# Optimization experiments

Measured on AMD Instinct MI355X. Metric: run time of the kernel, lower is better.

The kernel has to match this reference:

```python
import jax, jax.numpy as jnp
import numpy as np

B, M, H, E = 1, 2048, 16, 128
D = H * E          # 2048, model dim
C = 4 * D          # 8192, FFN dim
F = E
G = D
J = D


def setup_inputs() -> dict:
    key = jax.random.key(0)
    k_in, k_wv, k_wk, k_wq, k_wz, k_ffa, k_ffb = jax.random.split(key, 7)
    scale = 0.01
    return {
        "I_in": jax.random.normal(k_in, (B, M, D), dtype=jnp.float32),
        "WV": jax.random.normal(k_wv, (H, E, D), dtype=jnp.float32) * scale,
        "WK": jax.random.normal(k_wk, (H, E, D), dtype=jnp.float32) * scale,
        "WQ": jax.random.normal(k_wq, (H, E, D), dtype=jnp.float32) * scale,
        "WZ": jax.random.normal(k_wz, (H, F, G), dtype=jnp.float32) * scale,
        "WFFA": jax.random.normal(k_ffa, (G, C), dtype=jnp.float32) * scale,
        "WFFB": jax.random.normal(k_ffb, (C, J), dtype=jnp.float32) * scale,
    }


def reference(I_in, WV, WK, WQ, WZ, WFFA, WFFB):
    # QKV projections: [B,M,D] x [H,E,D] -> [B,M,H,E]
    V = jnp.einsum('bmd,hed->bmhe', I_in, WV)
    K = jnp.einsum('bmd,hed->bmhe', I_in, WK)
    Q = jnp.einsum('bmd,hed->bmhe', I_in, WQ)
    # Attention scores [B,M,P,H]; NOTE: no 1/sqrt(E) scaling in the original.
    QK = jnp.einsum('bmhe,bphe->bmph', Q, K)
    # Softmax over keys (p axis = 2), matching torch.softmax(QK, dim=2)
    QK_softmax = jax.nn.softmax(QK, axis=2)
    # Attention output [B,M,H,E]
    AV = jnp.einsum('bmph,bphe->bmhe', QK_softmax, V)
    # Output projection [B,M,G]
    Z = jnp.einsum('bmhf,hfg->bmg', AV, WZ)
    # FFN (no nonlinearity in the original workload)
    FFA = jnp.einsum('bmg,gc->bmc', Z, WFFA)
    FFB = jnp.einsum('bmc,cj->bmj', FFA, WFFB)
    return FFB
```

## Files before the change

kernel.cpp:

```cpp
#include <hip/hip_runtime.h>
#include <hip/hip_bf16.h>
#include <math.h>


typedef __bf16 bf16_t;
typedef __bf16 bf16x8 __attribute__((ext_vector_type(8)));
typedef float  f32x4  __attribute__((ext_vector_type(4)));

#define AS1 __attribute__((address_space(1)))
#define AS3 __attribute__((address_space(3)))

__device__ __forceinline__ void load16_lds(const bf16_t* g, bf16_t* l) {
    __builtin_amdgcn_global_load_lds((AS1 void*)g, (AS3 void*)l, 16, 0, 0);
}

template<typename TOUT, bool ATOMIC>
__global__ __launch_bounds__(256)
void gemm_bt(const bf16_t* __restrict__ A, const bf16_t* __restrict__ B,
             TOUT* __restrict__ Cc, int Mdim, int Ndim, int Kdim,
             int lda, int ldb, int ldc,
             long long ab, long long bb, long long cb,
             int ct_z, bf16_t* __restrict__ ctc, int ldct)
{
    __shared__ bf16_t As[128 * 32];
    __shared__ bf16_t Bs[128 * 32];

    const int z = blockIdx.z;
    A  += (long long)z * ab;
    B  += (long long)z * bb;
    Cc += (long long)z * cb;

    const int bm = blockIdx.y * 128;
    const int bn = blockIdx.x * 128;
    const int t  = threadIdx.x;
    const int lane = t & 63;
    const int w    = t >> 6;

    const int wm = (w & 1) * 64;
    const int wn = (w >> 1) * 64;

    const int sub = lane >> 2;
    const int seg = lane & 3;

    const bf16_t* Ag0 = A + (long long)(bm + w * 32 + sub) * lda + seg * 8;
    const bf16_t* Ag1 = Ag0 + 16LL * lda;
    const bf16_t* Bg0 = B + (long long)(bn + w * 32 + sub) * ldb + seg * 8;
    const bf16_t* Bg1 = Bg0 + 16LL * ldb;

    bf16_t* Al0 = &As[(w * 2 + 0) * 512];
    bf16_t* Al1 = &As[(w * 2 + 1) * 512];
    bf16_t* Bl0 = &Bs[(w * 2 + 0) * 512];
    bf16_t* Bl1 = &Bs[(w * 2 + 1) * 512];

    const int col  = lane & 15;
    const int koff = (lane >> 4) * 8;

    f32x4 acc[4][4] = {};

    for (int k0 = 0; k0 < Kdim; k0 += 32) {
        load16_lds(Ag0 + k0, Al0);
        load16_lds(Ag1 + k0, Al1);
        load16_lds(Bg0 + k0, Bl0);
        load16_lds(Bg1 + k0, Bl1);
        __syncthreads();

        bf16x8 af[4], bfr[4];
        #pragma unroll
        for (int mi = 0; mi < 4; ++mi)
            af[mi] = *(const bf16x8*)&As[(wm + mi * 16 + col) * 32 + koff];
        #pragma unroll
        for (int nj = 0; nj < 4; ++nj)
            bfr[nj] = *(const bf16x8*)&Bs[(wn + nj * 16 + col) * 32 + koff];
        #pragma unroll
        for (int mi = 0; mi < 4; ++mi)
            #pragma unroll
            for (int nj = 0; nj < 4; ++nj)
                acc[mi][nj] = __builtin_amdgcn_mfma_f32_16x16x32_bf16(
                    af[mi], bfr[nj], acc[mi][nj], 0, 0, 0);
        __syncthreads();
    }

    const int rbase = (lane >> 4) * 4;
    if (z == ct_z) {
        #pragma unroll
        for (int mi = 0; mi < 4; ++mi) {
            const long long mb = bm + wm + mi * 16 + rbase;
            #pragma unroll
            for (int nj = 0; nj < 4; ++nj) {
                const long long n = bn + wn + nj * 16 + col;
                union { bf16_t b[4]; unsigned long long u; } o;
                #pragma unroll
                for (int r = 0; r < 4; ++r) o.b[r] = (bf16_t)acc[mi][nj][r];
                *(unsigned long long*)(ctc + n * ldct + mb) = o.u;
            }
        }
    } else {
        #pragma unroll
        for (int mi = 0; mi < 4; ++mi) {
            #pragma unroll
            for (int r = 0; r < 4; ++r) {
                long long m = bm + wm + mi * 16 + rbase + r;
                TOUT* crow = Cc + m * ldc + bn + wn + col;
                #pragma unroll
                for (int nj = 0; nj < 4; ++nj) {
                    if constexpr (ATOMIC)
                        atomicAdd(&crow[nj * 16], (float)acc[mi][nj][r]);
                    else
                        crow[nj * 16] = (TOUT)acc[mi][nj][r];
                }
            }
        }
    }
}

__global__ __launch_bounds__(256, 2)
void flash_attn(const bf16_t* __restrict__ Q, const bf16_t* __restrict__ K,
                const bf16_t* __restrict__ VT, bf16_t* __restrict__ O,
                int M, int D)
{
    __shared__ bf16_t Kt[64 * 128];
    __shared__ bf16_t Vt[128 * 64];
    __shared__ bf16_t Pl[4 * 16 * 88];

    const int t = threadIdx.x, lane = t & 63, w = t >> 6;
    const int q4 = lane >> 4;
    const int c  = lane & 15;
    const int bm = blockIdx.x * 64;
    const int hE = blockIdx.y * 128;

    bf16x8 af_q[4];
    {
        const bf16_t* qrow = Q + (long long)(bm + w * 16 + c) * D + hE + q4 * 8;
        #pragma unroll
        for (int ks = 0; ks < 4; ++ks)
            af_q[ks] = *(const bf16x8*)(qrow + ks * 32);
    }

    f32x4 acc_o[8] = {};
    float m_i[4] = {-INFINITY, -INFINITY, -INFINITY, -INFINITY};
    float l_i[4] = {0.f, 0.f, 0.f, 0.f};

    bf16_t* Pw = &Pl[w * 16 * 88];

    for (int p0 = 0; p0 < M; p0 += 64) {
        #pragma unroll
        for (int j = 0; j < 4; ++j) {
            int krow = w * 16 + j * 4;
            load16_lds(K + (long long)(p0 + krow + q4) * D + hE + ((c ^ (j * 4 + q4)) * 8),
                       &Kt[krow * 128]);
            int vrow = w * 32 + j * 8;
            load16_lds(VT + (long long)(hE + vrow + (lane >> 3)) * M + p0
                          + (((lane & 7) ^ (lane >> 3)) * 8),
                       &Vt[vrow * 64]);
        }
        __syncthreads();

        f32x4 acc_s[4] = {};
        #pragma unroll
        for (int ks = 0; ks < 4; ++ks) {
            #pragma unroll
            for (int nj = 0; nj < 4; ++nj) {
                int row = nj * 16 + c;
                bf16x8 bk = *(const bf16x8*)&Kt[row * 128 + (((ks * 4 + q4) ^ c) * 8)];
                acc_s[nj] = __builtin_amdgcn_mfma_f32_16x16x32_bf16(
                    af_q[ks], bk, acc_s[nj], 0, 0, 0);
            }
        }

        float mt[4], alpha[4], rs[4];
        #pragma unroll
        for (int r = 0; r < 4; ++r) {
            float v = fmaxf(fmaxf(acc_s[0][r], acc_s[1][r]),
                            fmaxf(acc_s[2][r], acc_s[3][r]));
            #pragma unroll
            for (int off = 1; off < 16; off <<= 1)
                v = fmaxf(v, __shfl_xor(v, off));
            mt[r] = v;
        }
        #pragma unroll
        for (int r = 0; r < 4; ++r) {
            float mn = fmaxf(m_i[r], mt[r]);
            alpha[r] = __expf(m_i[r] - mn);
            m_i[r] = mn;
            rs[r] = 0.f;
        }
        #pragma unroll
        for (int nj = 0; nj < 4; ++nj)
            #pragma unroll
            for (int r = 0; r < 4; ++r) {
                float p = __expf(acc_s[nj][r] - m_i[r]);
                rs[r] += p;
                Pw[(q4 * 4 + r) * 88 + nj * 16 + c] = (bf16_t)p;
            }
        #pragma unroll
        for (int r = 0; r < 4; ++r) {
            float v = rs[r];
            #pragma unroll
            for (int off = 1; off < 16; off <<= 1)
                v += __shfl_xor(v, off);
            l_i[r] = alpha[r] * l_i[r] + v;
        }
        #pragma unroll
        for (int nj = 0; nj < 8; ++nj)
            #pragma unroll
            for (int r = 0; r < 4; ++r)
                acc_o[nj][r] *= alpha[r];
        __syncthreads();

        #pragma unroll
        for (int ks = 0; ks < 2; ++ks) {
            bf16x8 ap = *(const bf16x8*)&Pw[c * 88 + ks * 32 + q4 * 8];
            #pragma unroll
            for (int nj = 0; nj < 8; ++nj) {
                int row = nj * 16 + c;
                bf16x8 bv = *(const bf16x8*)&Vt[row * 64 + (((ks * 4 + q4) ^ (c & 7)) * 8)];
                acc_o[nj] = __builtin_amdgcn_mfma_f32_16x16x32_bf16(
                    ap, bv, acc_o[nj], 0, 0, 0);
            }
        }
        __syncthreads();
    }

    float inv[4];
    #pragma unroll
    for (int r = 0; r < 4; ++r) inv[r] = 1.0f / l_i[r];
    #pragma unroll
    for (int nj = 0; nj < 8; ++nj)
        #pragma unroll
        for (int r = 0; r < 4; ++r)
            O[(long long)(bm + w * 16 + q4 * 4 + r) * D + hE + nj * 16 + c] =
                (bf16_t)(acc_o[nj][r] * inv[r]);
}

__global__ __launch_bounds__(256)
void cast4_bf16(const float* __restrict__ s0, const float* __restrict__ s1,
                const float* __restrict__ s2, const float* __restrict__ s3,
                bf16_t* __restrict__ d0, long long seg, long long n)
{
    const float* src = (blockIdx.y == 0) ? s0 : (blockIdx.y == 1) ? s1
                     : (blockIdx.y == 2) ? s2 : s3;
    bf16_t* dst = d0 + (long long)blockIdx.y * seg;
    long long i = ((long long)blockIdx.x * 256 + threadIdx.x) * 4;
    if (i >= n) return;
    float4 v = *(const float4*)(src + i);
    union { bf16_t b[4]; unsigned long long u; } o;
    o.b[0] = (bf16_t)v.x; o.b[1] = (bf16_t)v.y;
    o.b[2] = (bf16_t)v.z; o.b[3] = (bf16_t)v.w;
    *(unsigned long long*)(dst + i) = o.u;
}

__global__ __launch_bounds__(256)
void transpose_to_bf16(const float* __restrict__ in, bf16_t* __restrict__ out,
                       int rows, int cols)
{
    __shared__ bf16_t tile[32][33];
    const int r0 = blockIdx.y * 32, c0 = blockIdx.x * 32;
    const int tx = threadIdx.x & 31, ty = threadIdx.x >> 5;
    #pragma unroll
    for (int i = 0; i < 4; ++i) {
        int r = ty + i * 8;
        tile[r][tx] = (bf16_t)in[(long long)(r0 + r) * cols + c0 + tx];
    }
    __syncthreads();
    #pragma unroll
    for (int i = 0; i < 4; ++i) {
        int r = ty + i * 8;
        out[(long long)(c0 + r) * rows + r0 + tx] = tile[tx][r];
    }
}

__global__ __launch_bounds__(256)
void zero_f32(float* __restrict__ p, long long n)
{
    long long i = ((long long)blockIdx.x * 256 + threadIdx.x) * 4;
    if (i >= n) return;
    *(float4*)(p + i) = float4{0.f, 0.f, 0.f, 0.f};
}

extern "C" void kernel_launch(void* const* d_in, const int* in_sizes, int n_in,
                              void* d_out, int out_size, void* d_ws, size_t ws_size,
                              hipStream_t stream)
{
    const float* I    = (const float*)d_in[0];
    const float* WV   = (const float*)d_in[1];
    const float* WK   = (const float*)d_in[2];
    const float* WQ   = (const float*)d_in[3];
    const float* WZ   = (const float*)d_in[4];
    const float* WFFA = (const float*)d_in[5];
    const float* WFFB = (const float*)d_in[6];
    float* out = (float*)d_out;

    const int M = 2048, D = 2048, C = 8192;
    const long long MD = (long long)M * D;
    const size_t MiB = 1024 * 1024;

    char* base = (char*)d_ws;
    bf16_t* bI     = (bf16_t*)(base + 0 * MiB);
    bf16_t* bWQ    = (bf16_t*)(base + 8 * MiB);
    bf16_t* bWK    = (bf16_t*)(base + 16 * MiB);
    bf16_t* bWV    = (bf16_t*)(base + 24 * MiB);
    bf16_t* bQ     = (bf16_t*)(base + 32 * MiB);
    bf16_t* bK     = (bf16_t*)(base + 40 * MiB);
    bf16_t* bVT    = (bf16_t*)(base + 48 * MiB);
    bf16_t* bAV    = (bf16_t*)(base + 56 * MiB);
    bf16_t* bZ     = (bf16_t*)(base + 64 * MiB);
    bf16_t* bWZT   = (bf16_t*)(base + 72 * MiB);
    bf16_t* bWFFAT = (bf16_t*)(base + 80 * MiB);
    bf16_t* bWFFBT = (bf16_t*)(base + 112 * MiB);
    bf16_t* bFFA   = (bf16_t*)(base + 0 * MiB);

    const dim3 blk(256);

    cast4_bf16<<<dim3(MD / 1024, 4), blk, 0, stream>>>(I, WQ, WK, WV, bI, MD, MD);
    transpose_to_bf16<<<dim3(D / 32, D / 32), blk, 0, stream>>>(WZ,   bWZT,   D, D);
    transpose_to_bf16<<<dim3(C / 32, D / 32), blk, 0, stream>>>(WFFA, bWFFAT, D, C);
    transpose_to_bf16<<<dim3(D / 32, C / 32), blk, 0, stream>>>(WFFB, bWFFBT, C, D);

    gemm_bt<bf16_t, false><<<dim3(16, 16, 3), blk, 0, stream>>>(
        bI, bWQ, bQ, M, D, D, D, D, D, 0, MD, MD, 2, bVT, M);

    flash_attn<<<dim3(M / 64, 16), blk, 0, stream>>>(bQ, bK, bVT, bAV, M, D);

    gemm_bt<bf16_t, false><<<dim3(16, 16, 1), blk, 0, stream>>>(
        bAV, bWZT, bZ, M, D, D, D, D, D, 0, 0, 0, -1, nullptr, 0);

    gemm_bt<bf16_t, false><<<dim3(64, 16, 1), blk, 0, stream>>>(
        bZ, bWFFAT, bFFA, M, C, D, D, D, C, 0, 0, 0, -1, nullptr, 0);

    zero_f32<<<dim3((int)(MD / 1024)), blk, 0, stream>>>(out, MD);
    gemm_bt<float, true><<<dim3(16, 16, 4), blk, 0, stream>>>(
        bFFA, bWFFBT, out, M, D, 2048, C, C, D, 2048, 2048, 0, -1, nullptr, 0);
}
```

Baseline: 690.3 us.

## Add 256x256 double-buffered GEMM kernel with swizzled LDS for large projections

Introduces a 512-thread GEMM kernel with 256x256 output tiles and 64-wide K steps. It double-buffers LDS, uses XOR-swizzled loads to avoid bank conflicts, and interleaves the next tile's async global-to-LDS loads with MFMA phases, raising MFMA priority during compute. The kernel replaces the 128x128 GEMM for the QKV, FFN-A and split-K FFN-B stages, aiming for more data reuse and better latency hiding. The cost is much more LDS (128KB per block) and more registers, which lowers occupancy and gives fewer blocks per grid (e.g. 192 for QKV).

```diff
diff --git a/kernel.cpp b/kernel.cpp
--- a/kernel.cpp
+++ b/kernel.cpp
@@ -12,6 +12,172 @@
 
 __device__ __forceinline__ void load16_lds(const bf16_t* g, bf16_t* l) {
     __builtin_amdgcn_global_load_lds((AS1 void*)g, (AS3 void*)l, 16, 0, 0);
+}
+
+
+__device__ __forceinline__ void stageA256(const bf16_t* __restrict__ Ab, int lda,
+                                          int k0, bf16_t* buf, int half,
+                                          int w, int lane)
+{
+    #pragma unroll
+    for (int j = 0; j < 2; ++j) {
+        const int prw = half * 128 + j * 64 + w * 8;
+        const int pr  = prw + (lane >> 3);
+        const int lr  = ((pr >> 6) & 1) * 128 + (pr >> 7) * 64 + (pr & 63);
+        const int lc  = (lane & 7) ^ (pr & 7);
+        load16_lds(Ab + (long long)lr * lda + k0 + lc * 8, buf + prw * 64);
+    }
+}
+
+__device__ __forceinline__ void stageB256(const bf16_t* __restrict__ Bb, int ldb,
+                                          int k0, bf16_t* buf, int half,
+                                          int w, int lane)
+{
+    #pragma unroll
+    for (int j = 0; j < 2; ++j) {
+        const int prw = half * 128 + j * 64 + w * 8;
+        const int pr  = prw + (lane >> 3);
+        const int lr  = ((pr >> 5) & 3) * 64 + (pr >> 7) * 32 + (pr & 31);
+        const int lc  = (lane & 7) ^ (pr & 7);
+        load16_lds(Bb + (long long)lr * ldb + k0 + lc * 8, buf + prw * 64);
+    }
+}
+
+#define G256_PHASE(MH, NH, DOA, DOB, STAGE, WAIT)                              \
+  {                                                                            \
+    if constexpr (DOA) {                                                       \
+      const int arow_ = (MH) * 128 + wm * 64 + (lane & 15);                    \
+      _Pragma("unroll")                                                        \
+      for (int ks = 0; ks < 2; ++ks) {                                         \
+        const int ch_ = (((ks * 4 + (lane >> 4)) ^ (lane & 7)) * 8);           \
+        _Pragma("unroll")                                                      \
+        for (int mi = 0; mi < 4; ++mi)                                         \
+          af[ks][mi] = *(const bf16x8*)&Ac[(arow_ + mi * 16) * 64 + ch_];      \
+      }                                                                        \
+    }                                                                          \
+    if constexpr (DOB) {                                                       \
+      const int brow_ = (NH) * 128 + wn * 32 + (lane & 15);                    \
+      _Pragma("unroll")                                                        \
+      for (int ks = 0; ks < 2; ++ks) {                                         \
+        const int ch_ = (((ks * 4 + (lane >> 4)) ^ (lane & 7)) * 8);           \
+        _Pragma("unroll")                                                      \
+        for (int nj = 0; nj < 2; ++nj)                                         \
+          bv[ks][nj] = *(const bf16x8*)&Bc[(brow_ + nj * 16) * 64 + ch_];      \
+      }                                                                        \
+    }                                                                          \
+    STAGE;                                                                     \
+    WAIT;                                                                      \
+    __builtin_amdgcn_s_barrier();                                              \
+    asm volatile("s_waitcnt lgkmcnt(0)" ::: "memory");                         \
+    __builtin_amdgcn_s_setprio(1);                                             \
+    _Pragma("unroll")                                                          \
+    for (int ks = 0; ks < 2; ++ks)                                             \
+      _Pragma("unroll")                                                        \
+      for (int mi = 0; mi < 4; ++mi)                                           \
+        _Pragma("unroll")                                                      \
+        for (int nj = 0; nj < 2; ++nj)                                         \
+          acc[(MH) * 4 + mi][(NH) * 2 + nj] =                                  \
+              __builtin_amdgcn_mfma_f32_16x16x32_bf16(                         \
+                  af[ks][mi], bv[ks][nj],                                      \
+                  acc[(MH) * 4 + mi][(NH) * 2 + nj], 0, 0, 0);                 \
+    __builtin_amdgcn_s_setprio(0);                                             \
+    __builtin_amdgcn_s_barrier();                                              \
+  }
+
+template<typename TOUT, bool ATOMIC>
+__global__ __launch_bounds__(512, 2)
+void gemm256_bt(const bf16_t* __restrict__ A, const bf16_t* __restrict__ B,
+                TOUT* __restrict__ Cc, int Kdim,
+                int lda, int ldb, int ldc,
+                long long ab, long long bb, long long cb,
+                int ct_z, bf16_t* __restrict__ ctc, int ldct)
+{
+    __shared__ __attribute__((aligned(16))) bf16_t Asl[2][256 * 64];
+    __shared__ __attribute__((aligned(16))) bf16_t Bsl[2][256 * 64];
+
+    const int z = blockIdx.z;
+    A  += (long long)z * ab;
+    B  += (long long)z * bb;
+    Cc += (long long)z * cb;
+
+    const int bm = blockIdx.y * 256;
+    const int bn = blockIdx.x * 256;
+    const int t = threadIdx.x, lane = t & 63, w = t >> 6;
+    const int wm = w >> 2, wn = w & 3;
+
+    const bf16_t* Ab = A + (long long)bm * lda;
+    const bf16_t* Bb = B + (long long)bn * ldb;
+
+    f32x4  acc[8][4] = {};
+    bf16x8 af[2][4];
+    bf16x8 bv[2][2];
+
+    stageA256(Ab, lda, 0, &Asl[0][0], 0, w, lane);
+    stageB256(Bb, ldb, 0, &Bsl[0][0], 0, w, lane);
+    stageA256(Ab, lda, 0, &Asl[0][0], 1, w, lane);
+    stageB256(Bb, ldb, 0, &Bsl[0][0], 1, w, lane);
+    asm volatile("s_waitcnt vmcnt(4)" ::: "memory");
+    __builtin_amdgcn_s_barrier();
+
+    const int NT = Kdim >> 6;
+    for (int kt = 0; kt < NT - 1; ++kt) {
+        const int cur = kt & 1, nxt = cur ^ 1;
+        const int k0n = (kt + 1) << 6;
+        const bf16_t* Ac = &Asl[cur][0];
+        const bf16_t* Bc = &Bsl[cur][0];
+        G256_PHASE(0, 0, 1, 1, stageA256(Ab, lda, k0n, &Asl[nxt][0], 0, w, lane),
+                   asm volatile("s_waitcnt vmcnt(4)" ::: "memory"));
+        G256_PHASE(1, 0, 1, 0, stageB256(Bb, ldb, k0n, &Bsl[nxt][0], 0, w, lane),
+                   asm volatile("s_waitcnt vmcnt(4)" ::: "memory"));
+        G256_PHASE(1, 1, 0, 1, stageA256(Ab, lda, k0n, &Asl[nxt][0], 1, w, lane),
+                   ((void)0));
+        G256_PHASE(0, 1, 1, 0, stageB256(Bb, ldb, k0n, &Bsl[nxt][0], 1, w, lane),
+                   asm volatile("s_waitcnt vmcnt(4)" ::: "memory"));
+    }
+    {
+        const int cur = (NT - 1) & 1;
+        const bf16_t* Ac = &Asl[cur][0];
+        const bf16_t* Bc = &Bsl[cur][0];
+        G256_PHASE(0, 0, 1, 1, ((void)0),
+                   asm volatile("s_waitcnt vmcnt(2)" ::: "memory"));
+        G256_PHASE(1, 0, 1, 0, ((void)0),
+                   asm volatile("s_waitcnt vmcnt(0)" ::: "memory"));
+        G256_PHASE(1, 1, 0, 1, ((void)0), ((void)0));
+        G256_PHASE(0, 1, 1, 0, ((void)0), ((void)0));
+    }
+
+    const int rb = (lane >> 4) * 4;
+    const int cc = lane & 15;
+    if (z == ct_z) {
+        #pragma unroll
+        for (int mi = 0; mi < 8; ++mi) {
+            const long long mb = bm + wm * 128 + mi * 16 + rb;
+            #pragma unroll
+            for (int nj = 0; nj < 4; ++nj) {
+                const long long n = bn + wn * 64 + nj * 16 + cc;
+                union { bf16_t b[4]; unsigned long long u; } o;
+                #pragma unroll
+                for (int r = 0; r < 4; ++r) o.b[r] = (bf16_t)acc[mi][nj][r];
+                *(unsigned long long*)(ctc + n * ldct + mb) = o.u;
+            }
+        }
+    } else {
+        #pragma unroll
+        for (int mi = 0; mi < 8; ++mi) {
+            #pragma unroll
+            for (int r = 0; r < 4; ++r) {
+                const long long m = bm + wm * 128 + mi * 16 + rb + r;
+                TOUT* crow = Cc + m * ldc + bn + wn * 64 + cc;
+                #pragma unroll
+                for (int nj = 0; nj < 4; ++nj) {
+                    if constexpr (ATOMIC)
+                        atomicAdd(&crow[nj * 16], (float)acc[mi][nj][r]);
+                    else
+                        crow[nj * 16] = (TOUT)acc[mi][nj][r];
+                }
+            }
+        }
+    }
 }
 
 template<typename TOUT, bool ATOMIC>
@@ -64,10 +230,10 @@
         load16_lds(Bg1 + k0, Bl1);
         __syncthreads();
 
-        bf16x8 af[4], bfr[4];
+        bf16x8 afr[4], bfr[4];
         #pragma unroll
         for (int mi = 0; mi < 4; ++mi)
-            af[mi] = *(const bf16x8*)&As[(wm + mi * 16 + col) * 32 + koff];
+            afr[mi] = *(const bf16x8*)&As[(wm + mi * 16 + col) * 32 + koff];
         #pragma unroll
         for (int nj = 0; nj < 4; ++nj)
             bfr[nj] = *(const bf16x8*)&Bs[(wn + nj * 16 + col) * 32 + koff];
@@ -76,7 +242,7 @@
             #pragma unroll
             for (int nj = 0; nj < 4; ++nj)
                 acc[mi][nj] = __builtin_amdgcn_mfma_f32_16x16x32_bf16(
-                    af[mi], bfr[nj], acc[mi][nj], 0, 0, 0);
+                    afr[mi], bfr[nj], acc[mi][nj], 0, 0, 0);
         __syncthreads();
     }
 
@@ -213,9 +379,9 @@
             #pragma unroll
             for (int nj = 0; nj < 8; ++nj) {
                 int row = nj * 16 + c;
-                bf16x8 bv = *(const bf16x8*)&Vt[row * 64 + (((ks * 4 + q4) ^ (c & 7)) * 8)];
+                bf16x8 bvv = *(const bf16x8*)&Vt[row * 64 + (((ks * 4 + q4) ^ (c & 7)) * 8)];
                 acc_o[nj] = __builtin_amdgcn_mfma_f32_16x16x32_bf16(
-                    ap, bv, acc_o[nj], 0, 0, 0);
+                    ap, bvv, acc_o[nj], 0, 0, 0);
             }
         }
         __syncthreads();
@@ -310,24 +476,25 @@
     bf16_t* bFFA   = (bf16_t*)(base + 0 * MiB);
 
     const dim3 blk(256);
+    const dim3 blk512(512);
 
     cast4_bf16<<<dim3(MD / 1024, 4), blk, 0, stream>>>(I, WQ, WK, WV, bI, MD, MD);
     transpose_to_bf16<<<dim3(D / 32, D / 32), blk, 0, stream>>>(WZ,   bWZT,   D, D);
     transpose_to_bf16<<<dim3(C / 32, D / 32), blk, 0, stream>>>(WFFA, bWFFAT, D, C);
     transpose_to_bf16<<<dim3(D / 32, C / 32), blk, 0, stream>>>(WFFB, bWFFBT, C, D);
 
-    gemm_bt<bf16_t, false><<<dim3(16, 16, 3), blk, 0, stream>>>(
-        bI, bWQ, bQ, M, D, D, D, D, D, 0, MD, MD, 2, bVT, M);
+    gemm256_bt<bf16_t, false><<<dim3(8, 8, 3), blk512, 0, stream>>>(
+        bI, bWQ, bQ, D, D, D, D, 0, MD, MD, 2, bVT, M);
 
     flash_attn<<<dim3(M / 64, 16), blk, 0, stream>>>(bQ, bK, bVT, bAV, M, D);
 
     gemm_bt<bf16_t, false><<<dim3(16, 16, 1), blk, 0, stream>>>(
         bAV, bWZT, bZ, M, D, D, D, D, D, 0, 0, 0, -1, nullptr, 0);
 
-    gemm_bt<bf16_t, false><<<dim3(64, 16, 1), blk, 0, stream>>>(
-        bZ, bWFFAT, bFFA, M, C, D, D, D, C, 0, 0, 0, -1, nullptr, 0);
+    gemm256_bt<bf16_t, false><<<dim3(32, 8, 1), blk512, 0, stream>>>(
+        bZ, bWFFAT, bFFA, D, D, D, C, 0, 0, 0, -1, nullptr, 0);
 
     zero_f32<<<dim3((int)(MD / 1024)), blk, 0, stream>>>(out, MD);
-    gemm_bt<float, true><<<dim3(16, 16, 4), blk, 0, stream>>>(
-        bFFA, bWFFBT, out, M, D, 2048, C, C, D, 2048, 2048, 0, -1, nullptr, 0);
-}
+    gemm256_bt<float, true><<<dim3(8, 8, 4), blk512, 0, stream>>>(
+        bFFA, bWFFBT, out, 2048, C, C, D, 2048, 2048, 0, -1, nullptr, 0);
+}
```

After: 691.7 us. Within noise of the previous version (+0.2%).

## Add 256x256 pipelined GEMM kernel and replace atomic split-K with partial-sum reduction

Applied to the files above, without the earlier changes.

Introduces a 512-thread GEMM with 256x256 tiles, K-step 64, XOR-swizzled LDS, multi-buffered async global-to-LDS staging with explicit vmcnt waits, and MFMA priority bumps. It is used for the QKV projection and both FFN GEMMs, cutting global and LDS traffic per FLOP and overlapping loads with compute. The FFB split-K no longer zeroes the output and accumulates atomically. It writes four fp32 partial buffers that a separate kernel sums, at the cost of extra workspace traffic. The larger tiles give fewer blocks (e.g. 192 or 256), which may leave some of the GPU's compute units underused.

```diff
diff --git a/kernel.cpp b/kernel.cpp
--- a/kernel.cpp
+++ b/kernel.cpp
@@ -12,6 +12,189 @@
 
 __device__ __forceinline__ void load16_lds(const bf16_t* g, bf16_t* l) {
     __builtin_amdgcn_global_load_lds((AS1 void*)g, (AS3 void*)l, 16, 0, 0);
+}
+
+__device__ __forceinline__ void stageA_half(const bf16_t* __restrict__ Ab, int lda,
+                                            int k0, int h, bf16_t* slot,
+                                            int w, int lane)
+{
+    #pragma unroll
+    for (int j = 0; j < 2; ++j) {
+        const int prw = j * 64 + w * 8;
+        const int p   = prw + (lane >> 3);
+        const int lr  = (p >> 6) * 128 + h * 64 + (p & 63);
+        const int lc  = (lane & 7) ^ (p & 7);
+        load16_lds(Ab + (long long)lr * lda + k0 + lc * 8, slot + prw * 64);
+    }
+}
+__device__ __forceinline__ void stageB_half(const bf16_t* __restrict__ Bb, int ldb,
+                                            int k0, int h, bf16_t* slot,
+                                            int w, int lane)
+{
+    #pragma unroll
+    for (int j = 0; j < 2; ++j) {
+        const int prw = j * 64 + w * 8;
+        const int p   = prw + (lane >> 3);
+        const int lr  = (p >> 5) * 64 + h * 32 + (p & 31);
+        const int lc  = (lane & 7) ^ (p & 7);
+        load16_lds(Bb + (long long)lr * ldb + k0 + lc * 8, slot + prw * 64);
+    }
+}
+
+#define LOADAF(SL)                                                             \
+  _Pragma("unroll") for (int ks = 0; ks < 2; ++ks)                             \
+  _Pragma("unroll") for (int mi = 0; mi < 4; ++mi)                             \
+      af[ks][mi] = *(const bf16x8*)&(SL)[(wm * 64 + mi * 16 + c15) * 64 +      \
+                      (((ks * 4 + q4) ^ (c15 & 7)) * 8)];
+
+#define LOADBV(DST, SL)                                                        \
+  _Pragma("unroll") for (int ks = 0; ks < 2; ++ks)                             \
+  _Pragma("unroll") for (int nj = 0; nj < 2; ++nj)                             \
+      DST[ks][nj] = *(const bf16x8*)&(SL)[(wn * 32 + nj * 16 + c15) * 64 +     \
+                      (((ks * 4 + q4) ^ (c15 & 7)) * 8)];
+
+#define MFMA16(MH, NH, BV)                                                     \
+  __builtin_amdgcn_s_setprio(1);                                               \
+  _Pragma("unroll") for (int ks = 0; ks < 2; ++ks)                             \
+  _Pragma("unroll") for (int mi = 0; mi < 4; ++mi)                             \
+  _Pragma("unroll") for (int nj = 0; nj < 2; ++nj)                             \
+      acc[(MH) * 4 + mi][(NH) * 2 + nj] =                                      \
+          __builtin_amdgcn_mfma_f32_16x16x32_bf16(                             \
+              af[ks][mi], BV[ks][nj], acc[(MH) * 4 + mi][(NH) * 2 + nj],       \
+              0, 0, 0);                                                        \
+  __builtin_amdgcn_s_setprio(0);
+
+#define VMW(N) asm volatile("s_waitcnt vmcnt(" #N ")" ::: "memory")
+#define BAR()  __builtin_amdgcn_s_barrier()
+
+template<typename TOUT>
+__global__ __launch_bounds__(512, 2)
+void gemm256d_bt(const bf16_t* __restrict__ A, const bf16_t* __restrict__ B,
+                 TOUT* __restrict__ Cc, int Kdim,
+                 int lda, int ldb, int ldc,
+                 long long ab, long long bb, long long cb,
+                 int ct_z, bf16_t* __restrict__ ctc, int ldct)
+{
+    __shared__ __attribute__((aligned(16))) bf16_t As[4][128 * 64];
+    __shared__ __attribute__((aligned(16))) bf16_t Bs[4][128 * 64];
+
+    const int z = blockIdx.z;
+    A  += (long long)z * ab;
+    B  += (long long)z * bb;
+    Cc += (long long)z * cb;
+
+    const int bm = blockIdx.y * 256;
+    const int bn = blockIdx.x * 256;
+    const int t = threadIdx.x, lane = t & 63, w = t >> 6;
+    const int wm = w >> 2, wn = w & 3;
+    const int q4 = lane >> 4, c15 = lane & 15;
+
+    const bf16_t* Ab = A + (long long)bm * lda;
+    const bf16_t* Bb = B + (long long)bn * ldb;
+
+    f32x4  acc[8][4] = {};
+    bf16x8 af[2][4];
+    bf16x8 bv0[2][2];
+    bf16x8 bv1[2][2];
+
+    stageA_half(Ab, lda, 0,  0, As[0], w, lane);
+    stageB_half(Bb, ldb, 0,  0, Bs[0], w, lane);
+    stageB_half(Bb, ldb, 0,  1, Bs[1], w, lane);
+    stageA_half(Ab, lda, 0,  1, As[1], w, lane);
+    stageA_half(Ab, lda, 64, 0, As[2], w, lane);
+    stageB_half(Bb, ldb, 64, 0, Bs[2], w, lane);
+    stageB_half(Bb, ldb, 64, 1, Bs[3], w, lane);
+
+    const int NT = Kdim >> 6;
+
+    for (int kt = 0; kt + 2 < NT; ++kt) {
+        const int par = kt & 1;
+        bf16_t* a0 = As[2 * par];
+        bf16_t* a1 = As[2 * par + 1];
+        bf16_t* b0 = Bs[2 * par];
+        bf16_t* b1 = Bs[2 * par + 1];
+        bf16_t* a1n = As[2 * (par ^ 1) + 1];
+        const int kn1 = (kt + 1) << 6, kn2 = (kt + 2) << 6;
+        VMW(10); BAR();
+        stageA_half(Ab, lda, kn1, 1, a1n, w, lane);
+        LOADAF(a0); LOADBV(bv0, b0);
+        MFMA16(0, 0, bv0);
+        VMW(10); BAR();
+        LOADBV(bv1, b1);
+        MFMA16(0, 1, bv1);
+        VMW(8); BAR();
+        stageA_half(Ab, lda, kn2, 0, a0, w, lane);
+        stageB_half(Bb, ldb, kn2, 0, b0, w, lane);
+        LOADAF(a1);
+        MFMA16(1, 1, bv1);
+        stageB_half(Bb, ldb, kn2, 1, b1, w, lane);
+        MFMA16(1, 0, bv0);
+    }
+    {
+        const int kt = NT - 2, par = kt & 1;
+        bf16_t* a0 = As[2 * par];
+        bf16_t* a1 = As[2 * par + 1];
+        bf16_t* b0 = Bs[2 * par];
+        bf16_t* b1 = Bs[2 * par + 1];
+        bf16_t* a1n = As[2 * (par ^ 1) + 1];
+        const int kn1 = (kt + 1) << 6;
+        VMW(10); BAR();
+        stageA_half(Ab, lda, kn1, 1, a1n, w, lane);
+        LOADAF(a0); LOADBV(bv0, b0);
+        MFMA16(0, 0, bv0);
+        VMW(10); BAR();
+        LOADBV(bv1, b1);
+        MFMA16(0, 1, bv1);
+        VMW(8); BAR();
+        LOADAF(a1);
+        MFMA16(1, 1, bv1);
+        MFMA16(1, 0, bv0);
+    }
+    {
+        const int par = (NT - 1) & 1;
+        bf16_t* a0 = As[2 * par];
+        bf16_t* a1 = As[2 * par + 1];
+        bf16_t* b0 = Bs[2 * par];
+        bf16_t* b1 = Bs[2 * par + 1];
+        VMW(4); BAR();
+        LOADAF(a0); LOADBV(bv0, b0);
+        MFMA16(0, 0, bv0);
+        VMW(2); BAR();
+        LOADBV(bv1, b1);
+        MFMA16(0, 1, bv1);
+        VMW(0); BAR();
+        LOADAF(a1);
+        MFMA16(1, 1, bv1);
+        MFMA16(1, 0, bv0);
+    }
+
+    const int rb = q4 * 4;
+    if (z == ct_z) {
+        #pragma unroll
+        for (int mi = 0; mi < 8; ++mi) {
+            const long long mb = bm + wm * 128 + mi * 16 + rb;
+            #pragma unroll
+            for (int nj = 0; nj < 4; ++nj) {
+                const long long n = bn + wn * 64 + nj * 16 + c15;
+                union { bf16_t b[4]; unsigned long long u; } o;
+                #pragma unroll
+                for (int r = 0; r < 4; ++r) o.b[r] = (bf16_t)acc[mi][nj][r];
+                *(unsigned long long*)(ctc + n * ldct + mb) = o.u;
+            }
+        }
+    } else {
+        #pragma unroll
+        for (int mi = 0; mi < 8; ++mi) {
+            #pragma unroll
+            for (int r = 0; r < 4; ++r) {
+                const long long m = bm + wm * 128 + mi * 16 + rb + r;
+                TOUT* crow = Cc + m * ldc + bn + wn * 64 + c15;
+                #pragma unroll
+                for (int nj = 0; nj < 4; ++nj)
+                    crow[nj * 16] = (TOUT)acc[mi][nj][r];
+            }
+        }
+    }
 }
 
 template<typename TOUT, bool ATOMIC>
@@ -22,8 +205,8 @@
              long long ab, long long bb, long long cb,
              int ct_z, bf16_t* __restrict__ ctc, int ldct)
 {
-    __shared__ bf16_t As[128 * 32];
-    __shared__ bf16_t Bs[128 * 32];
+    __shared__ bf16_t Ash[128 * 32];
+    __shared__ bf16_t Bsh[128 * 32];
 
     const int z = blockIdx.z;
     A  += (long long)z * ab;
@@ -47,10 +230,10 @@
     const bf16_t* Bg0 = B + (long long)(bn + w * 32 + sub) * ldb + seg * 8;
     const bf16_t* Bg1 = Bg0 + 16LL * ldb;
 
-    bf16_t* Al0 = &As[(w * 2 + 0) * 512];
-    bf16_t* Al1 = &As[(w * 2 + 1) * 512];
-    bf16_t* Bl0 = &Bs[(w * 2 + 0) * 512];
-    bf16_t* Bl1 = &Bs[(w * 2 + 1) * 512];
+    bf16_t* Al0 = &Ash[(w * 2 + 0) * 512];
+    bf16_t* Al1 = &Ash[(w * 2 + 1) * 512];
+    bf16_t* Bl0 = &Bsh[(w * 2 + 0) * 512];
+    bf16_t* Bl1 = &Bsh[(w * 2 + 1) * 512];
 
     const int col  = lane & 15;
     const int koff = (lane >> 4) * 8;
@@ -64,19 +247,19 @@
         load16_lds(Bg1 + k0, Bl1);
         __syncthreads();
 
-        bf16x8 af[4], bfr[4];
+        bf16x8 afr[4], bfr[4];
         #pragma unroll
         for (int mi = 0; mi < 4; ++mi)
-            af[mi] = *(const bf16x8*)&As[(wm + mi * 16 + col) * 32 + koff];
+            afr[mi] = *(const bf16x8*)&Ash[(wm + mi * 16 + col) * 32 + koff];
         #pragma unroll
         for (int nj = 0; nj < 4; ++nj)
-            bfr[nj] = *(const bf16x8*)&Bs[(wn + nj * 16 + col) * 32 + koff];
+            bfr[nj] = *(const bf16x8*)&Bsh[(wn + nj * 16 + col) * 32 + koff];
         #pragma unroll
         for (int mi = 0; mi < 4; ++mi)
             #pragma unroll
             for (int nj = 0; nj < 4; ++nj)
                 acc[mi][nj] = __builtin_amdgcn_mfma_f32_16x16x32_bf16(
-                    af[mi], bfr[nj], acc[mi][nj], 0, 0, 0);
+                    afr[mi], bfr[nj], acc[mi][nj], 0, 0, 0);
         __syncthreads();
     }
 
@@ -213,9 +396,9 @@
             #pragma unroll
             for (int nj = 0; nj < 8; ++nj) {
                 int row = nj * 16 + c;
-                bf16x8 bv = *(const bf16x8*)&Vt[row * 64 + (((ks * 4 + q4) ^ (c & 7)) * 8)];
+                bf16x8 bvv = *(const bf16x8*)&Vt[row * 64 + (((ks * 4 + q4) ^ (c & 7)) * 8)];
                 acc_o[nj] = __builtin_amdgcn_mfma_f32_16x16x32_bf16(
-                    ap, bv, acc_o[nj], 0, 0, 0);
+                    ap, bvv, acc_o[nj], 0, 0, 0);
             }
         }
         __syncthreads();
@@ -270,11 +453,21 @@
 }
 
 __global__ __launch_bounds__(256)
-void zero_f32(float* __restrict__ p, long long n)
+void reduce4_f32(const float* __restrict__ p, float* __restrict__ out,
+                 long long n)
 {
     long long i = ((long long)blockIdx.x * 256 + threadIdx.x) * 4;
     if (i >= n) return;
-    *(float4*)(p + i) = float4{0.f, 0.f, 0.f, 0.f};
+    float4 a = *(const float4*)(p + i);
+    float4 b = *(const float4*)(p + n + i);
+    float4 c = *(const float4*)(p + 2 * n + i);
+    float4 d = *(const float4*)(p + 3 * n + i);
+    float4 o;
+    o.x = a.x + b.x + c.x + d.x;
+    o.y = a.y + b.y + c.y + d.y;
+    o.z = a.z + b.z + c.z + d.z;
+    o.w = a.w + b.w + c.w + d.w;
+    *(float4*)(out + i) = o;
 }
 
 extern "C" void kernel_launch(void* const* d_in, const int* in_sizes, int n_in,
@@ -308,26 +501,29 @@
     bf16_t* bWFFAT = (bf16_t*)(base + 80 * MiB);
     bf16_t* bWFFBT = (bf16_t*)(base + 112 * MiB);
     bf16_t* bFFA   = (bf16_t*)(base + 0 * MiB);
+    float*  pF     = (float*)(base + 32 * MiB);
 
     const dim3 blk(256);
+    const dim3 blk512(512);
 
     cast4_bf16<<<dim3(MD / 1024, 4), blk, 0, stream>>>(I, WQ, WK, WV, bI, MD, MD);
     transpose_to_bf16<<<dim3(D / 32, D / 32), blk, 0, stream>>>(WZ,   bWZT,   D, D);
     transpose_to_bf16<<<dim3(C / 32, D / 32), blk, 0, stream>>>(WFFA, bWFFAT, D, C);
     transpose_to_bf16<<<dim3(D / 32, C / 32), blk, 0, stream>>>(WFFB, bWFFBT, C, D);
 
-    gemm_bt<bf16_t, false><<<dim3(16, 16, 3), blk, 0, stream>>>(
-        bI, bWQ, bQ, M, D, D, D, D, D, 0, MD, MD, 2, bVT, M);
+    gemm256d_bt<bf16_t><<<dim3(8, 8, 3), blk512, 0, stream>>>(
+        bI, bWQ, bQ, D, D, D, D, 0, MD, MD, 2, bVT, M);
 
     flash_attn<<<dim3(M / 64, 16), blk, 0, stream>>>(bQ, bK, bVT, bAV, M, D);
 
     gemm_bt<bf16_t, false><<<dim3(16, 16, 1), blk, 0, stream>>>(
         bAV, bWZT, bZ, M, D, D, D, D, D, 0, 0, 0, -1, nullptr, 0);
 
-    gemm_bt<bf16_t, false><<<dim3(64, 16, 1), blk, 0, stream>>>(
-        bZ, bWFFAT, bFFA, M, C, D, D, D, C, 0, 0, 0, -1, nullptr, 0);
-
-    zero_f32<<<dim3((int)(MD / 1024)), blk, 0, stream>>>(out, MD);
-    gemm_bt<float, true><<<dim3(16, 16, 4), blk, 0, stream>>>(
-        bFFA, bWFFBT, out, M, D, 2048, C, C, D, 2048, 2048, 0, -1, nullptr, 0);
-}
+    gemm256d_bt<bf16_t><<<dim3(32, 8, 1), blk512, 0, stream>>>(
+        bZ, bWFFAT, bFFA, D, D, D, C, 0, 0, 0, -1, nullptr, 0);
+
+    gemm256d_bt<float><<<dim3(8, 8, 4), blk512, 0, stream>>>(
+        bFFA, bWFFBT, pF, 2048, C, C, D, 2048, 2048, MD, -1, nullptr, 0);
+
+    reduce4_f32<<<dim3((int)(MD / 1024)), blk, 0, stream>>>(pF, out, MD);
+}
```

New measurement: 631.2 us. 1.09x faster.
